# Kernel tuning notes

Hardware: AMD Instinct MI355X
Metric: run time of the kernel (lower is better)

The kernel has to match this reference:

```python
import math
import jax, jax.numpy as jnp
import numpy as np

HEADS = 8
D_MODEL = 256


def positional_encoding_2d(c, h, w):
    # faithful port of wzlxjtu/PositionalEncoding2D
    d = c // 2
    div_term = jnp.exp(jnp.arange(0.0, d, 2, dtype=jnp.float32) * (-(math.log(10000.0) / d)))  # [d//2? no: d/2 entries -> d//2]
    pos_w = jnp.arange(0.0, w, dtype=jnp.float32)[:, None] * div_term  # [w, d//2]
    pos_h = jnp.arange(0.0, h, dtype=jnp.float32)[:, None] * div_term  # [h, d//2]
    pe = jnp.zeros((c, h, w), dtype=jnp.float32)
    sw = jnp.broadcast_to(jnp.sin(pos_w).T[:, None, :], (div_term.shape[0], h, w))
    cw = jnp.broadcast_to(jnp.cos(pos_w).T[:, None, :], (div_term.shape[0], h, w))
    sh = jnp.broadcast_to(jnp.sin(pos_h).T[:, :, None], (div_term.shape[0], h, w))
    ch = jnp.broadcast_to(jnp.cos(pos_h).T[:, :, None], (div_term.shape[0], h, w))
    pe = pe.at[0:d:2].set(sw)
    pe = pe.at[1:d:2].set(cw)
    pe = pe.at[d::2].set(sh)
    pe = pe.at[d + 1::2].set(ch)
    return pe


def setup_inputs() -> dict:
    key = jax.random.key(0)
    ks = jax.random.split(key, 9)
    b, c, h, w = 2, D_MODEL, 64, 64
    x = jax.random.normal(ks[0], (b, c, h, w), dtype=jnp.float32)
    s = 0.02
    Wq = jax.random.normal(ks[1], (c, c), dtype=jnp.float32) * s
    Wk = jax.random.normal(ks[2], (c, c), dtype=jnp.float32) * s
    Wv = jax.random.normal(ks[3], (c, c), dtype=jnp.float32) * s
    Wo = jax.random.normal(ks[4], (c, c), dtype=jnp.float32) * s
    bq = jax.random.normal(ks[5], (c,), dtype=jnp.float32) * s
    bk = jax.random.normal(ks[6], (c,), dtype=jnp.float32) * s
    bv = jax.random.normal(ks[7], (c,), dtype=jnp.float32) * s
    bo = jax.random.normal(ks[8], (c,), dtype=jnp.float32) * s
    return {"x": x, "Wq": Wq, "bq": bq, "Wk": Wk, "bk": bk,
            "Wv": Wv, "bv": bv, "Wo": Wo, "bo": bo}


def reference(x, Wq, bq, Wk, bk, Wv, bv, Wo, bo):
    b, c, h, w = x.shape
    dk = c // HEADS
    pe = positional_encoding_2d(c, h, w)
    x2 = x + pe[None]                                   # [b,c,h,w]
    tok = x2.reshape(b, c, h * w).transpose(0, 2, 1)    # [b,N,c]
    q = (tok @ Wq.T + bq).reshape(b, -1, HEADS, dk).transpose(0, 2, 1, 3)  # [b,H,N,dk]
    k = (tok @ Wk.T + bk).reshape(b, -1, HEADS, dk).transpose(0, 2, 1, 3)
    v = (tok @ Wv.T + bv).reshape(b, -1, HEADS, dk).transpose(0, 2, 1, 3)
    scores = jnp.einsum('bhnd,bhmd->bhnm', q, k) / math.sqrt(dk)  # [b,H,N,N]
    attn = jax.nn.softmax(scores, axis=-1)
    out = jnp.einsum('bhnm,bhmd->bhnd', attn, v)        # [b,H,N,dk]
    concat = out.transpose(0, 2, 1, 3).reshape(b, -1, c)  # [b,N,c]
    proj = concat @ Wo.T + bo                           # [b,N,c]
    return proj.transpose(0, 2, 1).reshape(b, c, h, w)
```

## Files before the change

### kernel.cpp

```cpp
#include <hip/hip_runtime.h>
#include <hip/hip_bf16.h>
#include <cstdint>

typedef float f32x4 __attribute__((ext_vector_type(4)));
typedef __bf16 bf16x8 __attribute__((ext_vector_type(8)));
typedef __bf16 bf16x4 __attribute__((ext_vector_type(4)));
typedef __bf16 bf16x2 __attribute__((ext_vector_type(2)));
typedef short short4v __attribute__((ext_vector_type(4)));
typedef uint32_t uint2v __attribute__((ext_vector_type(2)));

#define MFMA_K32(A, B, C) __builtin_amdgcn_mfma_f32_16x16x32_bf16((A), (B), (C), 0, 0, 0)

#if __has_builtin(__builtin_amdgcn_mfma_f32_16x16x16bf16_1k)
#define MFMA_K16(A, B, C) __builtin_amdgcn_mfma_f32_16x16x16bf16_1k((A), (B), (C), 0, 0, 0)
#elif __has_builtin(__builtin_amdgcn_mfma_f32_16x16x16_bf16)
static __device__ __forceinline__ f32x4 mfma_k16_alt(short4v a, short4v b, f32x4 c) {
    return __builtin_amdgcn_mfma_f32_16x16x16_bf16(*(bf16x4*)&a, *(bf16x4*)&b, c, 0, 0, 0);
}
#define MFMA_K16(A, B, C) mfma_k16_alt((A), (B), (C))
#else
#define MFMA_K16(A, B, C) (C)
#endif

#if __has_builtin(__builtin_amdgcn_exp2f)
#define EXP2(x) __builtin_amdgcn_exp2f(x)
#else
#define EXP2(x) exp2f(x)
#endif

static __device__ __forceinline__ uint16_t f2b(float f) {
    uint32_t u = __float_as_uint(f);
    uint32_t r = (u + 0x7fffu + ((u >> 16) & 1u)) >> 16;
    return (uint16_t)r;
}

static __device__ __forceinline__ uint32_t packbf(float a, float b) {
#if __has_builtin(__builtin_amdgcn_cvt_pk_bf16_f32)
    bf16x2 v = __builtin_amdgcn_cvt_pk_bf16_f32(a, b);
    return *(uint32_t*)&v;
#else
    uint32_t ua = __float_as_uint(a);
    ua += 0x7fffu + ((ua >> 16) & 1u);
    uint32_t ub = __float_as_uint(b);
    ub += 0x7fffu + ((ub >> 16) & 1u);
    return __builtin_amdgcn_perm(ub, ua, 0x07060302);
#endif
}

__global__ __launch_bounds__(256) void peadd(const float* __restrict__ x,
                                             uint16_t* __restrict__ tok) {
    __shared__ uint16_t T[64][65];
    int t = threadIdx.x, bid = blockIdx.x;
    int nt = bid & 63, ct = (bid >> 6) & 3, bb = bid >> 8;
    int n0 = nt << 6, c0 = ct << 6;
    int nl = t & 63, cq = t >> 6;
    int n = n0 + nl;
    float posh = (float)nt;
    float posw = (float)nl;
#pragma unroll
    for (int p = 0; p < 16; ++p) {
        int cl = cq * 16 + p;
        int cc = c0 + cl;
        int i = (cc & 127) >> 1;
        float dt = __expf((float)(2 * i) * -0.07195578415606394f);
        float sv, cv;
        __sincosf(((cc & 128) ? posh : posw) * dt, &sv, &cv);
        float pe = (cc & 1) ? cv : sv;
        T[cl][nl] = f2b(x[((size_t)(bb * 256 + cc) << 12) + n] + pe);
    }
    __syncthreads();
#pragma unroll
    for (int p = 0; p < 16; ++p) {
        int tl = cq * 16 + p;
        tok[(((size_t)(bb << 12) | (n0 + tl)) << 8) + c0 + nl] = T[nl][tl];
    }
}

__global__ __launch_bounds__(256) void qkv_gemm(const uint16_t* __restrict__ tok,
                                                const float* __restrict__ wqf,
                                                const float* __restrict__ wkf,
                                                const float* __restrict__ wvf,
                                                const float* __restrict__ bq,
                                                const float* __restrict__ bk,
                                                const float* __restrict__ bv,
                                                uint16_t* __restrict__ qo,
                                                uint16_t* __restrict__ ko,
                                                uint16_t* __restrict__ vo) {
    __shared__ __align__(16) uint16_t WS[64][264];
    __shared__ __align__(16) uint16_t VS[64][72];
    int tid = threadIdx.x, wvi = tid >> 6, lane = tid & 63;
    int c16 = lane & 15, quad = lane >> 4;
    int Mblk = blockIdx.x * 64;
    int M0 = Mblk + wvi * 16;
    int O0 = blockIdx.y * 64;
    const uint16_t* arow = tok + (size_t)(M0 + c16) * 256;
    bf16x8 af[8];
#pragma unroll
    for (int kk = 0; kk < 8; ++kk) af[kk] = *(const bf16x8*)(arow + kk * 32 + quad * 8);
    f32x4 zero = {0.f, 0.f, 0.f, 0.f};
    int bb = Mblk >> 12;
    int nloc = Mblk & 4095;
    int rt = tid >> 2, seg = tid & 3;
    for (int mat = 0; mat < 3; ++mat) {
        const float* Wg = ((mat == 0) ? wqf : (mat == 1) ? wkf : wvf) + (size_t)O0 * 256;
        __syncthreads();
#pragma unroll
        for (int p = 0; p < 16; ++p) {
            int idx = p * 1024 + tid * 4;
            f32x4 w4 = *(const f32x4*)(Wg + idx);
            uint2v pk;
            pk[0] = packbf(w4[0], w4[1]);
            pk[1] = packbf(w4[2], w4[3]);
            *(uint2v*)(&WS[idx >> 8][idx & 255]) = pk;
        }
        __syncthreads();
        f32x4 acc[4] = {zero, zero, zero, zero};
#pragma unroll
        for (int kk = 0; kk < 8; ++kk) {
            int k0 = kk * 32 + quad * 8;
#pragma unroll
            for (int nb = 0; nb < 4; ++nb)
                acc[nb] = MFMA_K32(*(const bf16x8*)(&WS[nb * 16 + c16][k0]),
                                   af[kk], acc[nb]);
        }
        if (mat < 2) {
            const float* bias = (mat == 0) ? bq : bk;
            float scale = (mat == 0) ? 0.25505654134660127f : 1.0f;
#pragma unroll
            for (int nb = 0; nb < 4; ++nb) {
                int o = O0 + nb * 16 + quad * 4;
                f32x4 bi = *(const f32x4*)(bias + o);
                uint2v pk;
                pk[0] = packbf((acc[nb][0] + bi[0]) * scale, (acc[nb][1] + bi[1]) * scale);
                pk[1] = packbf((acc[nb][2] + bi[2]) * scale, (acc[nb][3] + bi[3]) * scale);
                *(uint2v*)(&VS[wvi * 16 + c16][nb * 16 + quad * 4]) = pk;
            }
            __syncthreads();
            uint16_t* dst = (mat == 0) ? qo : ko;
            int o0 = O0 + seg * 16;
            int h = o0 >> 5, d0 = o0 & 31;
            size_t addr = ((size_t)(bb * 8 + h) * 4096 + nloc + rt) * 32 + d0;
            *(bf16x8*)(dst + addr) = *(const bf16x8*)(&VS[rt][seg * 16]);
            *(bf16x8*)(dst + addr + 8) = *(const bf16x8*)(&VS[rt][seg * 16 + 8]);
        } else {
            const float* bias = bv;
#pragma unroll
            for (int nb = 0; nb < 4; ++nb)
#pragma unroll
                for (int r = 0; r < 4; ++r) {
                    int o = O0 + nb * 16 + quad * 4 + r;
                    VS[nb * 16 + quad * 4 + r][wvi * 16 + c16] = f2b(acc[nb][r] + bias[o]);
                }
            __syncthreads();
            int o = O0 + rt;
            size_t addr = ((size_t)(bb * 8 + (o >> 5)) * 32 + (o & 31)) * 4096 + nloc + seg * 16;
            *(bf16x8*)(vo + addr) = *(const bf16x8*)(&VS[rt][seg * 16]);
            *(bf16x8*)(vo + addr + 8) = *(const bf16x8*)(&VS[rt][seg * 16 + 8]);
        }
    }
}

static __device__ __forceinline__ void attn_qblock(const bf16x8 (&kf)[4],
                                                   const short4v (&vf)[2][4],
                                                   bf16x8 qf, f32x4& oA, f32x4& oB,
                                                   f32x4& oS) {
    f32x4 zero = {0.f, 0.f, 0.f, 0.f};
    const short4v ones = {0x3F80, 0x3F80, 0x3F80, 0x3F80};
    f32x4 s[4];
#pragma unroll
    for (int kc = 0; kc < 4; ++kc) s[kc] = MFMA_K32(kf[kc], qf, zero);
#pragma unroll
    for (int kc = 0; kc < 4; ++kc) {
#pragma unroll
        for (int r = 0; r < 4; ++r) s[kc][r] = EXP2(s[kc][r]);
        union { short4v s4; uint32_t u[2]; } pa;
        pa.u[0] = packbf(s[kc][0], s[kc][1]);
        pa.u[1] = packbf(s[kc][2], s[kc][3]);
        oA = MFMA_K16(pa.s4, vf[0][kc], oA);
        oB = MFMA_K16(pa.s4, vf[1][kc], oB);
        oS = MFMA_K16(pa.s4, ones, oS);
    }
}

__global__ __launch_bounds__(512, 4) void flash(const uint16_t* __restrict__ qb,
                                                const uint16_t* __restrict__ kb,
                                                const uint16_t* __restrict__ vtb,
                                                uint16_t* __restrict__ concat) {
    __shared__ __align__(16) char smem[38912];
    int tid = threadIdx.x, wv = tid >> 6, lane = tid & 63;
    int c16 = lane & 15, quad = lane >> 4;
    int half = tid >> 8, t2 = tid & 255;
    int bh = blockIdx.y;
    int q0 = (blockIdx.x << 7) + (wv & 3) * 32;
    size_t base = (size_t)bh << 12;

    uint16_t* KT = (uint16_t*)(smem + half * 19456);
    uint16_t* VT = (uint16_t*)(smem + half * 19456 + 10240);

    const uint16_t* kgp = kb + (base + (size_t)half * 2048 + (t2 >> 2)) * 32 + (t2 & 3) * 8;
    const uint16_t* vgp = vtb + ((size_t)bh * 32 + (t2 >> 3)) * 4096 + half * 2048 + (t2 & 7) * 8;
    uint16_t* kls = KT + (t2 >> 2) * 40 + (t2 & 3) * 8;
    uint16_t* vls = VT + (t2 >> 3) * 72 + (t2 & 7) * 8;

    bf16x8 qf0 = *(const bf16x8*)(qb + (base + q0 + c16) * 32 + quad * 8);
    bf16x8 qf1 = *(const bf16x8*)(qb + (base + q0 + 16 + c16) * 32 + quad * 8);

    f32x4 zero = {0.f, 0.f, 0.f, 0.f};
    f32x4 o00 = zero, o01 = zero, o10 = zero, o11 = zero;
    f32x4 oS0 = zero, oS1 = zero;

    {
        bf16x8 kr = *(const bf16x8*)kgp;
        bf16x8 vr = *(const bf16x8*)vgp;
        *(bf16x8*)kls = kr;
        *(bf16x8*)vls = vr;
    }
    __syncthreads();

    for (int kt = 0; kt < 32; ++kt) {
        int cur = kt & 1;
        int kn = (kt + 1) & 31;
        bf16x8 kr = *(const bf16x8*)(kgp + (size_t)kn * 2048);
        bf16x8 vr = *(const bf16x8*)(vgp + kn * 64);
        const uint16_t* kfp = KT + cur * 2560 + c16 * 40 + quad * 8;
        const uint16_t* vfp = VT + cur * 2304 + c16 * 72 + quad * 4;
        bf16x8 kf[4];
        short4v vf[2][4];
#pragma unroll
        for (int kc = 0; kc < 4; ++kc) kf[kc] = *(const bf16x8*)(kfp + kc * 640);
#pragma unroll
        for (int kc = 0; kc < 4; ++kc) {
            vf[0][kc] = *(const short4v*)(vfp + kc * 16);
            vf[1][kc] = *(const short4v*)(vfp + 1152 + kc * 16);
        }
        attn_qblock(kf, vf, qf0, o00, o01, oS0);
        attn_qblock(kf, vf, qf1, o10, o11, oS1);
        *(bf16x8*)(kls + (cur ^ 1) * 2560) = kr;
        *(bf16x8*)(vls + (cur ^ 1) * 2304) = vr;
        __syncthreads();
    }

    float* ov = (float*)smem;
    if (wv >= 4) {
        float* d = ov + ((wv - 4) * 64 + lane) * 25;
#pragma unroll
        for (int r = 0; r < 4; ++r) {
            d[r] = o00[r]; d[4 + r] = o01[r]; d[8 + r] = o10[r]; d[12 + r] = o11[r];
            d[16 + r] = oS0[r]; d[20 + r] = oS1[r];
        }
    }
    __syncthreads();
    if (wv < 4) {
        const float* s = ov + (wv * 64 + lane) * 25;
#pragma unroll
        for (int r = 0; r < 4; ++r) {
            o00[r] += s[r]; o01[r] += s[4 + r]; o10[r] += s[8 + r]; o11[r] += s[12 + r];
            oS0[r] += s[16 + r]; oS1[r] += s[20 + r];
        }
        int h = bh & 7, bb = bh >> 3;
#pragma unroll
        for (int r = 0; r < 4; ++r) {
            float i0 = 1.f / oS0[r];
            float i1 = 1.f / oS1[r];
            int n = q0 + quad * 4 + r;
            size_t row0 = ((size_t)bb * 4096 + n) * 256 + h * 32;
            size_t row1 = ((size_t)bb * 4096 + n + 16) * 256 + h * 32;
            concat[row0 + c16]      = f2b(o00[r] * i0);
            concat[row0 + 16 + c16] = f2b(o01[r] * i0);
            concat[row1 + c16]      = f2b(o10[r] * i1);
            concat[row1 + 16 + c16] = f2b(o11[r] * i1);
        }
    }
}

__global__ __launch_bounds__(256) void proj_gemm(const uint16_t* __restrict__ concat,
                                                 const float* __restrict__ wof,
                                                 const float* __restrict__ bo,
                                                 float* __restrict__ out) {
    __shared__ __align__(16) uint16_t WS[64][264];
    int tid = threadIdx.x, wvi = tid >> 6, lane = tid & 63;
    int c16 = lane & 15, quad = lane >> 4;
    int M0 = blockIdx.x * 64 + wvi * 16;
    int O0 = blockIdx.y * 64;
    const float* Wg = wof + (size_t)O0 * 256;
#pragma unroll
    for (int p = 0; p < 16; ++p) {
        int idx = p * 1024 + tid * 4;
        f32x4 w4 = *(const f32x4*)(Wg + idx);
        uint2v pk;
        pk[0] = packbf(w4[0], w4[1]);
        pk[1] = packbf(w4[2], w4[3]);
        *(uint2v*)(&WS[idx >> 8][idx & 255]) = pk;
    }
    const uint16_t* crow = concat + (size_t)(M0 + c16) * 256;
    bf16x8 af[8];
#pragma unroll
    for (int kk = 0; kk < 8; ++kk) af[kk] = *(const bf16x8*)(crow + kk * 32 + quad * 8);
    __syncthreads();
    f32x4 zero = {0.f, 0.f, 0.f, 0.f};
    f32x4 acc[4] = {zero, zero, zero, zero};
#pragma unroll
    for (int kk = 0; kk < 8; ++kk) {
        int k0 = kk * 32 + quad * 8;
#pragma unroll
        for (int nb = 0; nb < 4; ++nb)
            acc[nb] = MFMA_K32(*(const bf16x8*)(&WS[nb * 16 + c16][k0]),
                               af[kk], acc[nb]);
    }
    int bb = M0 >> 12, n = (M0 + c16) & 4095;
#pragma unroll
    for (int nb = 0; nb < 4; ++nb)
#pragma unroll
        for (int r = 0; r < 4; ++r) {
            int o = O0 + nb * 16 + quad * 4 + r;
            out[((size_t)(bb * 256 + o) << 12) + n] = acc[nb][r] + bo[o];
        }
}

extern "C" void kernel_launch(void* const* d_in, const int* in_sizes, int n_in,
                              void* d_out, int out_size, void* d_ws, size_t ws_size,
                              hipStream_t stream) {
    const float* x  = (const float*)d_in[0];
    const float* Wq = (const float*)d_in[1];
    const float* bq = (const float*)d_in[2];
    const float* Wk = (const float*)d_in[3];
    const float* bk = (const float*)d_in[4];
    const float* Wv = (const float*)d_in[5];
    const float* bv = (const float*)d_in[6];
    const float* Wo = (const float*)d_in[7];
    const float* bo = (const float*)d_in[8];
    float* out = (float*)d_out;

    uint16_t* ws   = (uint16_t*)d_ws;
    uint16_t* tok  = ws;
    uint16_t* q    = tok + 2097152;
    uint16_t* k    = q + 2097152;
    uint16_t* vt   = k + 2097152;
    uint16_t* cc   = vt + 2097152;

    peadd<<<512, 256, 0, stream>>>(x, tok);
    qkv_gemm<<<dim3(128, 4), 256, 0, stream>>>(tok, Wq, Wk, Wv, bq, bk, bv, q, k, vt);
    flash<<<dim3(32, 16), 512, 0, stream>>>(q, k, vt, cc);
    proj_gemm<<<dim3(128, 4), 256, 0, stream>>>(cc, Wo, bo, out);
}
```

Measured before the change: 153.2 us.

## Fuse PE-add into QKV GEMM and split flash KV across four wave groups

Removes the separate positional-encoding kernel: the QKV GEMM now computes x+PE itself and stages the bf16 token tile in shared memory, so the intermediate token buffer is never written or read. Each block in the flash kernel now covers 64 queries instead of 128, and the KV sequence is split into four partitions reduced through shared memory, which doubles the grid and raises the occupancy hint. The projection GEMM stages its A tile through shared memory with coalesced loads. In exchange, the QKV blocks repeat the PE sin/exp work for every output-column block (4x), and the flash kernel adds reduction overhead.

```diff
diff --git a/kernel.cpp b/kernel.cpp
--- a/kernel.cpp
+++ b/kernel.cpp
@@ -47,59 +47,52 @@
 #endif
 }
 
-__global__ __launch_bounds__(256) void peadd(const float* __restrict__ x,
-                                             uint16_t* __restrict__ tok) {
-    __shared__ uint16_t T[64][65];
-    int t = threadIdx.x, bid = blockIdx.x;
-    int nt = bid & 63, ct = (bid >> 6) & 3, bb = bid >> 8;
-    int n0 = nt << 6, c0 = ct << 6;
-    int nl = t & 63, cq = t >> 6;
-    int n = n0 + nl;
-    float posh = (float)nt;
-    float posw = (float)nl;
-#pragma unroll
-    for (int p = 0; p < 16; ++p) {
-        int cl = cq * 16 + p;
-        int cc = c0 + cl;
-        int i = (cc & 127) >> 1;
-        float dt = __expf((float)(2 * i) * -0.07195578415606394f);
-        float sv, cv;
-        __sincosf(((cc & 128) ? posh : posw) * dt, &sv, &cv);
-        float pe = (cc & 1) ? cv : sv;
-        T[cl][nl] = f2b(x[((size_t)(bb * 256 + cc) << 12) + n] + pe);
-    }
-    __syncthreads();
-#pragma unroll
-    for (int p = 0; p < 16; ++p) {
-        int tl = cq * 16 + p;
-        tok[(((size_t)(bb << 12) | (n0 + tl)) << 8) + c0 + nl] = T[nl][tl];
-    }
-}
-
-__global__ __launch_bounds__(256) void qkv_gemm(const uint16_t* __restrict__ tok,
-                                                const float* __restrict__ wqf,
-                                                const float* __restrict__ wkf,
-                                                const float* __restrict__ wvf,
-                                                const float* __restrict__ bq,
-                                                const float* __restrict__ bk,
-                                                const float* __restrict__ bv,
-                                                uint16_t* __restrict__ qo,
-                                                uint16_t* __restrict__ ko,
-                                                uint16_t* __restrict__ vo) {
-    __shared__ __align__(16) uint16_t WS[64][264];
+__global__ __launch_bounds__(256) void qkv_fused(const float* __restrict__ x,
+                                                 const float* __restrict__ wqf,
+                                                 const float* __restrict__ wkf,
+                                                 const float* __restrict__ wvf,
+                                                 const float* __restrict__ bq,
+                                                 const float* __restrict__ bk,
+                                                 const float* __restrict__ bv,
+                                                 uint16_t* __restrict__ qo,
+                                                 uint16_t* __restrict__ ko,
+                                                 uint16_t* __restrict__ vo) {
+    __shared__ __align__(16) char ubuf[33792];
     __shared__ __align__(16) uint16_t VS[64][72];
+    uint16_t (*AT)[264] = (uint16_t(*)[264])ubuf;
+    uint16_t (*WS)[264] = (uint16_t(*)[264])ubuf;
     int tid = threadIdx.x, wvi = tid >> 6, lane = tid & 63;
     int c16 = lane & 15, quad = lane >> 4;
     int Mblk = blockIdx.x * 64;
-    int M0 = Mblk + wvi * 16;
     int O0 = blockIdx.y * 64;
-    const uint16_t* arow = tok + (size_t)(M0 + c16) * 256;
+    int bb = Mblk >> 12, nloc = Mblk & 4095;
+    int nl = tid & 63, cq = tid >> 6;
+    int tokloc = nloc + nl;
+    float posw = (float)(tokloc & 63), posh = (float)((tokloc >> 6) & 63);
+#pragma unroll
+    for (int j = 0; j < 16; ++j) {
+        int cc = cq * 64 + j * 4;
+        float v[4];
+#pragma unroll
+        for (int e = 0; e < 4; ++e) {
+            int c = cc + e;
+            int i = (c & 127) >> 1;
+            float dt = __expf((float)(2 * i) * -0.07195578415606394f);
+            float sv, cvv;
+            __sincosf(((c & 128) ? posh : posw) * dt, &sv, &cvv);
+            v[e] = x[((size_t)(bb * 256 + c) << 12) + tokloc] + ((c & 1) ? cvv : sv);
+        }
+        uint2v pk;
+        pk[0] = packbf(v[0], v[1]);
+        pk[1] = packbf(v[2], v[3]);
+        *(uint2v*)(&AT[nl][cc]) = pk;
+    }
+    __syncthreads();
     bf16x8 af[8];
 #pragma unroll
-    for (int kk = 0; kk < 8; ++kk) af[kk] = *(const bf16x8*)(arow + kk * 32 + quad * 8);
+    for (int kk = 0; kk < 8; ++kk)
+        af[kk] = *(const bf16x8*)(&AT[wvi * 16 + c16][kk * 32 + quad * 8]);
     f32x4 zero = {0.f, 0.f, 0.f, 0.f};
-    int bb = Mblk >> 12;
-    int nloc = Mblk & 4095;
     int rt = tid >> 2, seg = tid & 3;
     for (int mat = 0; mat < 3; ++mat) {
         const float* Wg = ((mat == 0) ? wqf : (mat == 1) ? wkf : wvf) + (size_t)O0 * 256;
@@ -160,17 +153,17 @@
     }
 }
 
-static __device__ __forceinline__ void attn_qblock(const bf16x8 (&kf)[4],
-                                                   const short4v (&vf)[2][4],
+static __device__ __forceinline__ void attn_qblock(const bf16x8 (&kf)[2],
+                                                   const short4v (&vf)[2][2],
                                                    bf16x8 qf, f32x4& oA, f32x4& oB,
                                                    f32x4& oS) {
     f32x4 zero = {0.f, 0.f, 0.f, 0.f};
     const short4v ones = {0x3F80, 0x3F80, 0x3F80, 0x3F80};
-    f32x4 s[4];
-#pragma unroll
-    for (int kc = 0; kc < 4; ++kc) s[kc] = MFMA_K32(kf[kc], qf, zero);
-#pragma unroll
-    for (int kc = 0; kc < 4; ++kc) {
+    f32x4 s[2];
+#pragma unroll
+    for (int kc = 0; kc < 2; ++kc) s[kc] = MFMA_K32(kf[kc], qf, zero);
+#pragma unroll
+    for (int kc = 0; kc < 2; ++kc) {
 #pragma unroll
         for (int r = 0; r < 4; ++r) s[kc][r] = EXP2(s[kc][r]);
         union { short4v s4; uint32_t u[2]; } pa;
@@ -182,25 +175,26 @@
     }
 }
 
-__global__ __launch_bounds__(512, 4) void flash(const uint16_t* __restrict__ qb,
+__global__ __launch_bounds__(512, 6) void flash(const uint16_t* __restrict__ qb,
                                                 const uint16_t* __restrict__ kb,
                                                 const uint16_t* __restrict__ vtb,
                                                 uint16_t* __restrict__ concat) {
-    __shared__ __align__(16) char smem[38912];
+    __shared__ __align__(16) char smem[40960];
     int tid = threadIdx.x, wv = tid >> 6, lane = tid & 63;
     int c16 = lane & 15, quad = lane >> 4;
-    int half = tid >> 8, t2 = tid & 255;
+    int qr = tid >> 7, qt = tid & 127;
+    int qstrip = wv & 1;
     int bh = blockIdx.y;
-    int q0 = (blockIdx.x << 7) + (wv & 3) * 32;
+    int q0 = (blockIdx.x << 6) + qstrip * 32;
     size_t base = (size_t)bh << 12;
 
-    uint16_t* KT = (uint16_t*)(smem + half * 19456);
-    uint16_t* VT = (uint16_t*)(smem + half * 19456 + 10240);
-
-    const uint16_t* kgp = kb + (base + (size_t)half * 2048 + (t2 >> 2)) * 32 + (t2 & 3) * 8;
-    const uint16_t* vgp = vtb + ((size_t)bh * 32 + (t2 >> 3)) * 4096 + half * 2048 + (t2 & 7) * 8;
-    uint16_t* kls = KT + (t2 >> 2) * 40 + (t2 & 3) * 8;
-    uint16_t* vls = VT + (t2 >> 3) * 72 + (t2 & 7) * 8;
+    uint16_t* KTq = (uint16_t*)(smem + qr * 10240);
+    uint16_t* VTq = KTq + 2560;
+
+    const uint16_t* kgp = kb + (base + qr * 1024 + (qt >> 2)) * 32 + (qt & 3) * 8;
+    const uint16_t* vgp = vtb + ((size_t)bh * 32 + (qt >> 2)) * 4096 + qr * 1024 + (qt & 3) * 8;
+    uint16_t* kls = KTq + (qt >> 2) * 40 + (qt & 3) * 8;
+    uint16_t* vls = VTq + (qt >> 2) * 40 + (qt & 3) * 8;
 
     bf16x8 qf0 = *(const bf16x8*)(qb + (base + q0 + c16) * 32 + quad * 8);
     bf16x8 qf1 = *(const bf16x8*)(qb + (base + q0 + 16 + c16) * 32 + quad * 8);
@@ -209,53 +203,59 @@
     f32x4 o00 = zero, o01 = zero, o10 = zero, o11 = zero;
     f32x4 oS0 = zero, oS1 = zero;
 
-    {
-        bf16x8 kr = *(const bf16x8*)kgp;
-        bf16x8 vr = *(const bf16x8*)vgp;
-        *(bf16x8*)kls = kr;
-        *(bf16x8*)vls = vr;
-    }
+    *(bf16x8*)kls = *(const bf16x8*)kgp;
+    *(bf16x8*)vls = *(const bf16x8*)vgp;
     __syncthreads();
 
     for (int kt = 0; kt < 32; ++kt) {
         int cur = kt & 1;
         int kn = (kt + 1) & 31;
-        bf16x8 kr = *(const bf16x8*)(kgp + (size_t)kn * 2048);
-        bf16x8 vr = *(const bf16x8*)(vgp + kn * 64);
-        const uint16_t* kfp = KT + cur * 2560 + c16 * 40 + quad * 8;
-        const uint16_t* vfp = VT + cur * 2304 + c16 * 72 + quad * 4;
-        bf16x8 kf[4];
-        short4v vf[2][4];
-#pragma unroll
-        for (int kc = 0; kc < 4; ++kc) kf[kc] = *(const bf16x8*)(kfp + kc * 640);
-#pragma unroll
-        for (int kc = 0; kc < 4; ++kc) {
-            vf[0][kc] = *(const short4v*)(vfp + kc * 16);
-            vf[1][kc] = *(const short4v*)(vfp + 1152 + kc * 16);
-        }
+        bf16x8 kr = *(const bf16x8*)(kgp + (size_t)kn * 1024);
+        bf16x8 vr = *(const bf16x8*)(vgp + kn * 32);
+        const uint16_t* kfp = KTq + cur * 1280 + c16 * 40 + quad * 8;
+        const uint16_t* vfp = VTq + cur * 1280 + c16 * 40 + quad * 4;
+        bf16x8 kf[2];
+        short4v vf[2][2];
+        kf[0] = *(const bf16x8*)(kfp);
+        kf[1] = *(const bf16x8*)(kfp + 640);
+        vf[0][0] = *(const short4v*)(vfp);
+        vf[0][1] = *(const short4v*)(vfp + 16);
+        vf[1][0] = *(const short4v*)(vfp + 640);
+        vf[1][1] = *(const short4v*)(vfp + 656);
         attn_qblock(kf, vf, qf0, o00, o01, oS0);
         attn_qblock(kf, vf, qf1, o10, o11, oS1);
-        *(bf16x8*)(kls + (cur ^ 1) * 2560) = kr;
-        *(bf16x8*)(vls + (cur ^ 1) * 2304) = vr;
+        *(bf16x8*)(kls + (cur ^ 1) * 1280) = kr;
+        *(bf16x8*)(vls + (cur ^ 1) * 1280) = vr;
         __syncthreads();
     }
 
     float* ov = (float*)smem;
-    if (wv >= 4) {
-        float* d = ov + ((wv - 4) * 64 + lane) * 25;
+    if (wv >= 2) {
+        float* d = ov + (size_t)(wv - 2) * 24 * 64 + lane;
 #pragma unroll
         for (int r = 0; r < 4; ++r) {
-            d[r] = o00[r]; d[4 + r] = o01[r]; d[8 + r] = o10[r]; d[12 + r] = o11[r];
-            d[16 + r] = oS0[r]; d[20 + r] = oS1[r];
-        }
-    }
-    __syncthreads();
-    if (wv < 4) {
-        const float* s = ov + (wv * 64 + lane) * 25;
-#pragma unroll
-        for (int r = 0; r < 4; ++r) {
-            o00[r] += s[r]; o01[r] += s[4 + r]; o10[r] += s[8 + r]; o11[r] += s[12 + r];
-            oS0[r] += s[16 + r]; oS1[r] += s[20 + r];
+            d[(0 * 4 + r) * 64] = o00[r];
+            d[(1 * 4 + r) * 64] = o01[r];
+            d[(2 * 4 + r) * 64] = o10[r];
+            d[(3 * 4 + r) * 64] = o11[r];
+            d[(4 * 4 + r) * 64] = oS0[r];
+            d[(5 * 4 + r) * 64] = oS1[r];
+        }
+    }
+    __syncthreads();
+    if (wv < 2) {
+#pragma unroll
+        for (int part = 0; part < 3; ++part) {
+            const float* s = ov + (size_t)(part * 2 + wv) * 24 * 64 + lane;
+#pragma unroll
+            for (int r = 0; r < 4; ++r) {
+                o00[r] += s[(0 * 4 + r) * 64];
+                o01[r] += s[(1 * 4 + r) * 64];
+                o10[r] += s[(2 * 4 + r) * 64];
+                o11[r] += s[(3 * 4 + r) * 64];
+                oS0[r] += s[(4 * 4 + r) * 64];
+                oS1[r] += s[(5 * 4 + r) * 64];
+            }
         }
         int h = bh & 7, bb = bh >> 3;
 #pragma unroll
@@ -273,15 +273,29 @@
     }
 }
 
-__global__ __launch_bounds__(256) void proj_gemm(const uint16_t* __restrict__ concat,
-                                                 const float* __restrict__ wof,
-                                                 const float* __restrict__ bo,
-                                                 float* __restrict__ out) {
-    __shared__ __align__(16) uint16_t WS[64][264];
+__global__ __launch_bounds__(256) void proj_fused(const uint16_t* __restrict__ concat,
+                                                  const float* __restrict__ wof,
+                                                  const float* __restrict__ bo,
+                                                  float* __restrict__ out) {
+    __shared__ __align__(16) char ubuf[33792];
+    uint16_t (*AT)[264] = (uint16_t(*)[264])ubuf;
+    uint16_t (*WS)[264] = (uint16_t(*)[264])ubuf;
     int tid = threadIdx.x, wvi = tid >> 6, lane = tid & 63;
     int c16 = lane & 15, quad = lane >> 4;
-    int M0 = blockIdx.x * 64 + wvi * 16;
+    int Mblk = blockIdx.x * 64;
     int O0 = blockIdx.y * 64;
+#pragma unroll
+    for (int p = 0; p < 8; ++p) {
+        int idx = p * 2048 + tid * 8;
+        *(bf16x8*)(&AT[idx >> 8][idx & 255]) =
+            *(const bf16x8*)(concat + (size_t)Mblk * 256 + idx);
+    }
+    __syncthreads();
+    bf16x8 af[8];
+#pragma unroll
+    for (int kk = 0; kk < 8; ++kk)
+        af[kk] = *(const bf16x8*)(&AT[wvi * 16 + c16][kk * 32 + quad * 8]);
+    __syncthreads();
     const float* Wg = wof + (size_t)O0 * 256;
 #pragma unroll
     for (int p = 0; p < 16; ++p) {
@@ -292,10 +306,6 @@
         pk[1] = packbf(w4[2], w4[3]);
         *(uint2v*)(&WS[idx >> 8][idx & 255]) = pk;
     }
-    const uint16_t* crow = concat + (size_t)(M0 + c16) * 256;
-    bf16x8 af[8];
-#pragma unroll
-    for (int kk = 0; kk < 8; ++kk) af[kk] = *(const bf16x8*)(crow + kk * 32 + quad * 8);
     __syncthreads();
     f32x4 zero = {0.f, 0.f, 0.f, 0.f};
     f32x4 acc[4] = {zero, zero, zero, zero};
@@ -307,7 +317,7 @@
             acc[nb] = MFMA_K32(*(const bf16x8*)(&WS[nb * 16 + c16][k0]),
                                af[kk], acc[nb]);
     }
-    int bb = M0 >> 12, n = (M0 + c16) & 4095;
+    int bb = Mblk >> 12, n = (Mblk + wvi * 16 + c16) & 4095;
 #pragma unroll
     for (int nb = 0; nb < 4; ++nb)
 #pragma unroll
@@ -332,14 +342,12 @@
     float* out = (float*)d_out;
 
     uint16_t* ws   = (uint16_t*)d_ws;
-    uint16_t* tok  = ws;
-    uint16_t* q    = tok + 2097152;
+    uint16_t* q    = ws;
     uint16_t* k    = q + 2097152;
     uint16_t* vt   = k + 2097152;
     uint16_t* cc   = vt + 2097152;
 
-    peadd<<<512, 256, 0, stream>>>(x, tok);
-    qkv_gemm<<<dim3(128, 4), 256, 0, stream>>>(tok, Wq, Wk, Wv, bq, bk, bv, q, k, vt);
-    flash<<<dim3(32, 16), 512, 0, stream>>>(q, k, vt, cc);
-    proj_gemm<<<dim3(128, 4), 256, 0, stream>>>(cc, Wo, bo, out);
-}
+    qkv_fused<<<dim3(128, 4), 256, 0, stream>>>(x, Wq, Wk, Wv, bq, bk, bv, q, k, vt);
+    flash<<<dim3(64, 16), 512, 0, stream>>>(q, k, vt, cc);
+    proj_fused<<<dim3(128, 4), 256, 0, stream>>>(cc, Wo, bo, out);
+}
```

Measured after the change: 160.8 us. 1.05x slower.

## Preconvert weights to bf16 in prep kernel and stage GEMM A tiles through LDS

Applied to the files above, without the earlier changes.

Adds a prep kernel that converts all four weight matrices to bf16 once, alongside the positional-encoding add, so the GEMM blocks load bf16 weights directly and skip repeated fp32-to-bf16 conversion. The QKV and projection GEMMs now load their activation tile coalesced into LDS before building the fragments. Q and K are written straight to global memory without the LDS transpose. The flash attention loop is manually unrolled by two to use constant buffer indices. The cost is extra launch blocks, a workspace region for the bf16 weights, and narrower scattered global stores for Q and K.

```diff
diff --git a/kernel.cpp b/kernel.cpp
--- a/kernel.cpp
+++ b/kernel.cpp
@@ -47,11 +47,24 @@
 #endif
 }
 
-__global__ __launch_bounds__(256) void peadd(const float* __restrict__ x,
-                                             uint16_t* __restrict__ tok) {
+__global__ __launch_bounds__(256) void prep(const float* __restrict__ wq,
+                                            const float* __restrict__ wk,
+                                            const float* __restrict__ wv,
+                                            const float* __restrict__ wo,
+                                            const float* __restrict__ x,
+                                            uint16_t* __restrict__ Wb,
+                                            uint16_t* __restrict__ tok) {
+    int bid = blockIdx.x, t = threadIdx.x;
+    if (bid < 1024) {
+        int idx = bid * 256 + t;
+        int which = idx >> 16, off = idx & 65535;
+        const float* s = (which == 0) ? wq : (which == 1) ? wk : (which == 2) ? wv : wo;
+        Wb[idx] = f2b(s[off]);
+        return;
+    }
     __shared__ uint16_t T[64][65];
-    int t = threadIdx.x, bid = blockIdx.x;
-    int nt = bid & 63, ct = (bid >> 6) & 3, bb = bid >> 8;
+    int pb = bid - 1024;
+    int nt = pb & 63, ct = (pb >> 6) & 3, bb = pb >> 8;
     int n0 = nt << 6, c0 = ct << 6;
     int nl = t & 63, cq = t >> 6;
     int n = n0 + nl;
@@ -77,41 +90,44 @@
 }
 
 __global__ __launch_bounds__(256) void qkv_gemm(const uint16_t* __restrict__ tok,
-                                                const float* __restrict__ wqf,
-                                                const float* __restrict__ wkf,
-                                                const float* __restrict__ wvf,
+                                                const uint16_t* __restrict__ Wall,
                                                 const float* __restrict__ bq,
                                                 const float* __restrict__ bk,
                                                 const float* __restrict__ bv,
                                                 uint16_t* __restrict__ qo,
                                                 uint16_t* __restrict__ ko,
                                                 uint16_t* __restrict__ vo) {
-    __shared__ __align__(16) uint16_t WS[64][264];
+    __shared__ __align__(16) char ubuf[33792];
     __shared__ __align__(16) uint16_t VS[64][72];
+    uint16_t (*AT)[264] = (uint16_t(*)[264])ubuf;
+    uint16_t (*WS)[264] = (uint16_t(*)[264])ubuf;
     int tid = threadIdx.x, wvi = tid >> 6, lane = tid & 63;
     int c16 = lane & 15, quad = lane >> 4;
     int Mblk = blockIdx.x * 64;
     int M0 = Mblk + wvi * 16;
     int O0 = blockIdx.y * 64;
-    const uint16_t* arow = tok + (size_t)(M0 + c16) * 256;
+    int bb = M0 >> 12, n = (M0 + c16) & 4095;
+    int nloc = Mblk & 4095;
+#pragma unroll
+    for (int p = 0; p < 8; ++p) {
+        int idx = p * 2048 + tid * 8;
+        *(bf16x8*)(&AT[idx >> 8][idx & 255]) =
+            *(const bf16x8*)(tok + (size_t)Mblk * 256 + idx);
+    }
+    __syncthreads();
     bf16x8 af[8];
 #pragma unroll
-    for (int kk = 0; kk < 8; ++kk) af[kk] = *(const bf16x8*)(arow + kk * 32 + quad * 8);
+    for (int kk = 0; kk < 8; ++kk)
+        af[kk] = *(const bf16x8*)(&AT[wvi * 16 + c16][kk * 32 + quad * 8]);
     f32x4 zero = {0.f, 0.f, 0.f, 0.f};
-    int bb = Mblk >> 12;
-    int nloc = Mblk & 4095;
     int rt = tid >> 2, seg = tid & 3;
     for (int mat = 0; mat < 3; ++mat) {
-        const float* Wg = ((mat == 0) ? wqf : (mat == 1) ? wkf : wvf) + (size_t)O0 * 256;
+        const uint16_t* Wg = Wall + (size_t)mat * 65536 + (size_t)O0 * 256;
         __syncthreads();
 #pragma unroll
-        for (int p = 0; p < 16; ++p) {
-            int idx = p * 1024 + tid * 4;
-            f32x4 w4 = *(const f32x4*)(Wg + idx);
-            uint2v pk;
-            pk[0] = packbf(w4[0], w4[1]);
-            pk[1] = packbf(w4[2], w4[3]);
-            *(uint2v*)(&WS[idx >> 8][idx & 255]) = pk;
+        for (int p = 0; p < 8; ++p) {
+            int idx = p * 2048 + tid * 8;
+            *(bf16x8*)(&WS[idx >> 8][idx & 255]) = *(const bf16x8*)(Wg + idx);
         }
         __syncthreads();
         f32x4 acc[4] = {zero, zero, zero, zero};
@@ -126,30 +142,24 @@
         if (mat < 2) {
             const float* bias = (mat == 0) ? bq : bk;
             float scale = (mat == 0) ? 0.25505654134660127f : 1.0f;
+            uint16_t* dst = (mat == 0) ? qo : ko;
 #pragma unroll
             for (int nb = 0; nb < 4; ++nb) {
                 int o = O0 + nb * 16 + quad * 4;
                 f32x4 bi = *(const f32x4*)(bias + o);
+                int h = o >> 5, dd = o & 31;
                 uint2v pk;
                 pk[0] = packbf((acc[nb][0] + bi[0]) * scale, (acc[nb][1] + bi[1]) * scale);
                 pk[1] = packbf((acc[nb][2] + bi[2]) * scale, (acc[nb][3] + bi[3]) * scale);
-                *(uint2v*)(&VS[wvi * 16 + c16][nb * 16 + quad * 4]) = pk;
+                *(uint2v*)(dst + ((size_t)(bb * 8 + h) * 4096 + n) * 32 + dd) = pk;
             }
-            __syncthreads();
-            uint16_t* dst = (mat == 0) ? qo : ko;
-            int o0 = O0 + seg * 16;
-            int h = o0 >> 5, d0 = o0 & 31;
-            size_t addr = ((size_t)(bb * 8 + h) * 4096 + nloc + rt) * 32 + d0;
-            *(bf16x8*)(dst + addr) = *(const bf16x8*)(&VS[rt][seg * 16]);
-            *(bf16x8*)(dst + addr + 8) = *(const bf16x8*)(&VS[rt][seg * 16 + 8]);
         } else {
-            const float* bias = bv;
 #pragma unroll
             for (int nb = 0; nb < 4; ++nb)
 #pragma unroll
                 for (int r = 0; r < 4; ++r) {
                     int o = O0 + nb * 16 + quad * 4 + r;
-                    VS[nb * 16 + quad * 4 + r][wvi * 16 + c16] = f2b(acc[nb][r] + bias[o]);
+                    VS[nb * 16 + quad * 4 + r][wvi * 16 + c16] = f2b(acc[nb][r] + bv[o]);
                 }
             __syncthreads();
             int o = O0 + rt;
@@ -209,36 +219,35 @@
     f32x4 o00 = zero, o01 = zero, o10 = zero, o11 = zero;
     f32x4 oS0 = zero, oS1 = zero;
 
-    {
-        bf16x8 kr = *(const bf16x8*)kgp;
-        bf16x8 vr = *(const bf16x8*)vgp;
-        *(bf16x8*)kls = kr;
-        *(bf16x8*)vls = vr;
-    }
-    __syncthreads();
-
-    for (int kt = 0; kt < 32; ++kt) {
-        int cur = kt & 1;
-        int kn = (kt + 1) & 31;
-        bf16x8 kr = *(const bf16x8*)(kgp + (size_t)kn * 2048);
-        bf16x8 vr = *(const bf16x8*)(vgp + kn * 64);
-        const uint16_t* kfp = KT + cur * 2560 + c16 * 40 + quad * 8;
-        const uint16_t* vfp = VT + cur * 2304 + c16 * 72 + quad * 4;
-        bf16x8 kf[4];
-        short4v vf[2][4];
-#pragma unroll
-        for (int kc = 0; kc < 4; ++kc) kf[kc] = *(const bf16x8*)(kfp + kc * 640);
-#pragma unroll
-        for (int kc = 0; kc < 4; ++kc) {
-            vf[0][kc] = *(const short4v*)(vfp + kc * 16);
-            vf[1][kc] = *(const short4v*)(vfp + 1152 + kc * 16);
-        }
-        attn_qblock(kf, vf, qf0, o00, o01, oS0);
-        attn_qblock(kf, vf, qf1, o10, o11, oS1);
-        *(bf16x8*)(kls + (cur ^ 1) * 2560) = kr;
-        *(bf16x8*)(vls + (cur ^ 1) * 2304) = vr;
-        __syncthreads();
-    }
+    *(bf16x8*)kls = *(const bf16x8*)kgp;
+    *(bf16x8*)vls = *(const bf16x8*)vgp;
+    __syncthreads();
+
+#define FSTEP(CUR, KN)                                                        \
+    {                                                                         \
+        bf16x8 kr = *(const bf16x8*)(kgp + (size_t)(KN) * 2048);              \
+        bf16x8 vr = *(const bf16x8*)(vgp + (KN) * 64);                        \
+        const uint16_t* kfp = KT + (CUR) * 2560 + c16 * 40 + quad * 8;        \
+        const uint16_t* vfp = VT + (CUR) * 2304 + c16 * 72 + quad * 4;        \
+        bf16x8 kf[4];                                                         \
+        short4v vf[2][4];                                                     \
+        _Pragma("unroll") for (int kc = 0; kc < 4; ++kc)                      \
+            kf[kc] = *(const bf16x8*)(kfp + kc * 640);                        \
+        _Pragma("unroll") for (int kc = 0; kc < 4; ++kc) {                    \
+            vf[0][kc] = *(const short4v*)(vfp + kc * 16);                     \
+            vf[1][kc] = *(const short4v*)(vfp + 1152 + kc * 16);              \
+        }                                                                     \
+        attn_qblock(kf, vf, qf0, o00, o01, oS0);                              \
+        attn_qblock(kf, vf, qf1, o10, o11, oS1);                              \
+        *(bf16x8*)(kls + (1 - (CUR)) * 2560) = kr;                            \
+        *(bf16x8*)(vls + (1 - (CUR)) * 2304) = vr;                            \
+        __syncthreads();                                                      \
+    }
+    for (int i2 = 0; i2 < 16; ++i2) {
+        FSTEP(0, 2 * i2 + 1)
+        FSTEP(1, (2 * i2 + 2) & 31)
+    }
+#undef FSTEP
 
     float* ov = (float*)smem;
     if (wv >= 4) {
@@ -274,28 +283,34 @@
 }
 
 __global__ __launch_bounds__(256) void proj_gemm(const uint16_t* __restrict__ concat,
-                                                 const float* __restrict__ wof,
+                                                 const uint16_t* __restrict__ Wob,
                                                  const float* __restrict__ bo,
                                                  float* __restrict__ out) {
-    __shared__ __align__(16) uint16_t WS[64][264];
+    __shared__ __align__(16) char ubuf[33792];
+    uint16_t (*AT)[264] = (uint16_t(*)[264])ubuf;
+    uint16_t (*WS)[264] = (uint16_t(*)[264])ubuf;
     int tid = threadIdx.x, wvi = tid >> 6, lane = tid & 63;
     int c16 = lane & 15, quad = lane >> 4;
-    int M0 = blockIdx.x * 64 + wvi * 16;
+    int Mblk = blockIdx.x * 64;
     int O0 = blockIdx.y * 64;
-    const float* Wg = wof + (size_t)O0 * 256;
-#pragma unroll
-    for (int p = 0; p < 16; ++p) {
-        int idx = p * 1024 + tid * 4;
-        f32x4 w4 = *(const f32x4*)(Wg + idx);
-        uint2v pk;
-        pk[0] = packbf(w4[0], w4[1]);
-        pk[1] = packbf(w4[2], w4[3]);
-        *(uint2v*)(&WS[idx >> 8][idx & 255]) = pk;
-    }
-    const uint16_t* crow = concat + (size_t)(M0 + c16) * 256;
+#pragma unroll
+    for (int p = 0; p < 8; ++p) {
+        int idx = p * 2048 + tid * 8;
+        *(bf16x8*)(&AT[idx >> 8][idx & 255]) =
+            *(const bf16x8*)(concat + (size_t)Mblk * 256 + idx);
+    }
+    __syncthreads();
     bf16x8 af[8];
 #pragma unroll
-    for (int kk = 0; kk < 8; ++kk) af[kk] = *(const bf16x8*)(crow + kk * 32 + quad * 8);
+    for (int kk = 0; kk < 8; ++kk)
+        af[kk] = *(const bf16x8*)(&AT[wvi * 16 + c16][kk * 32 + quad * 8]);
+    __syncthreads();
+    const uint16_t* Wg = Wob + (size_t)O0 * 256;
+#pragma unroll
+    for (int p = 0; p < 8; ++p) {
+        int idx = p * 2048 + tid * 8;
+        *(bf16x8*)(&WS[idx >> 8][idx & 255]) = *(const bf16x8*)(Wg + idx);
+    }
     __syncthreads();
     f32x4 zero = {0.f, 0.f, 0.f, 0.f};
     f32x4 acc[4] = {zero, zero, zero, zero};
@@ -307,7 +322,7 @@
             acc[nb] = MFMA_K32(*(const bf16x8*)(&WS[nb * 16 + c16][k0]),
                                af[kk], acc[nb]);
     }
-    int bb = M0 >> 12, n = (M0 + c16) & 4095;
+    int bb = Mblk >> 12, n = (Mblk + wvi * 16 + c16) & 4095;
 #pragma unroll
     for (int nb = 0; nb < 4; ++nb)
 #pragma unroll
@@ -332,14 +347,15 @@
     float* out = (float*)d_out;
 
     uint16_t* ws   = (uint16_t*)d_ws;
-    uint16_t* tok  = ws;
+    uint16_t* Wb   = ws;
+    uint16_t* tok  = Wb + 262144;
     uint16_t* q    = tok + 2097152;
     uint16_t* k    = q + 2097152;
     uint16_t* vt   = k + 2097152;
     uint16_t* cc   = vt + 2097152;
 
-    peadd<<<512, 256, 0, stream>>>(x, tok);
-    qkv_gemm<<<dim3(128, 4), 256, 0, stream>>>(tok, Wq, Wk, Wv, bq, bk, bv, q, k, vt);
+    prep<<<1536, 256, 0, stream>>>(Wq, Wk, Wv, Wo, x, Wb, tok);
+    qkv_gemm<<<dim3(128, 4), 256, 0, stream>>>(tok, Wb, bq, bk, bv, q, k, vt);
     flash<<<dim3(32, 16), 512, 0, stream>>>(q, k, vt, cc);
-    proj_gemm<<<dim3(128, 4), 256, 0, stream>>>(cc, Wo, bo, out);
-}
+    proj_gemm<<<dim3(128, 4), 256, 0, stream>>>(cc, Wb + 3 * 65536, bo, out);
+}
```

Result: no change. 152.5 us (-0.5%).
